# Performance work log

Measured on AMD Instinct MI355X. Metric: run time of the kernel, lower is better.

The kernel has to match this reference:

```python
import jax, jax.numpy as jnp
import numpy as np

D_MODEL = 1024
NUM_HEADS = 16
D_K = D_MODEL // NUM_HEADS  # 64
THETA = 10000.0


def apply_rope(x, positions, theta):
    # x: [b, h, s, d_k]; interleaved-pair RoPE
    d = x.shape[-1]
    inv_freq = theta ** (-jnp.arange(0, d, 2, dtype=jnp.float32) / d)  # [d/2]
    angles = positions.astype(jnp.float32)[:, None] * inv_freq[None, :]  # [s, d/2]
    cos = jnp.cos(angles)
    sin = jnp.sin(angles)
    x1 = x[..., 0::2]
    x2 = x[..., 1::2]
    out_even = x1 * cos - x2 * sin
    out_odd = x1 * sin + x2 * cos
    return jnp.stack([out_even, out_odd], axis=-1).reshape(x.shape)


def setup_inputs() -> dict:
    key = jax.random.key(0)
    kx, kq, kk, kv, ko = jax.random.split(key, 5)
    scale = 1.0 / np.sqrt(D_MODEL)
    return {
        "x": jax.random.normal(kx, (1, 4096, D_MODEL), dtype=jnp.float32),
        "Wq": jax.random.normal(kq, (D_MODEL, D_MODEL), dtype=jnp.float32) * scale,
        "Wk": jax.random.normal(kk, (D_MODEL, D_MODEL), dtype=jnp.float32) * scale,
        "Wv": jax.random.normal(kv, (D_MODEL, D_MODEL), dtype=jnp.float32) * scale,
        "Wo": jax.random.normal(ko, (D_MODEL, D_MODEL), dtype=jnp.float32) * scale,
    }


def reference(x, Wq, Wk, Wv, Wo):
    b, s, _ = x.shape
    # Linear (no bias, weight stored as [out, in]): y = x @ W^T
    q = jnp.einsum("bsd,ed->bse", x, Wq).reshape(b, s, NUM_HEADS, D_K).transpose(0, 2, 1, 3)
    k = jnp.einsum("bsd,ed->bse", x, Wk).reshape(b, s, NUM_HEADS, D_K).transpose(0, 2, 1, 3)
    v = jnp.einsum("bsd,ed->bse", x, Wv).reshape(b, s, NUM_HEADS, D_K).transpose(0, 2, 1, 3)

    positions = jnp.arange(s)
    q = apply_rope(q, positions, THETA)
    k = apply_rope(k, positions, THETA)

    scores = jnp.einsum("bhqd,bhkd->bhqk", q, k) / jnp.sqrt(jnp.float32(D_K))
    causal = jnp.tril(jnp.ones((s, s), dtype=bool))
    scores = jnp.where(causal, scores, -jnp.inf)
    probs = jax.nn.softmax(scores, axis=-1)
    ctx = jnp.einsum("bhqk,bhkd->bhqd", probs, v)  # [b,h,s,d_k]
    ctx = ctx.transpose(0, 2, 1, 3).reshape(b, s, D_MODEL)
    return jnp.einsum("bse,de->bsd", ctx, Wo)
```

## Files before the change

kernel.cpp:

```cpp
#include <hip/hip_runtime.h>
#include <hip/hip_bf16.h>
#include <math.h>


#define S_LEN 4096
#define DMODEL 1024
#define NHEAD 16
#define QSCALE 0.1803368801111244f

typedef __attribute__((ext_vector_type(8))) short short8;
typedef __attribute__((ext_vector_type(4))) short short4_t;
typedef __attribute__((ext_vector_type(4))) float floatx4;

static __device__ __forceinline__ void load_lds16(const void* g, void* l) {
    __builtin_amdgcn_global_load_lds((const __attribute__((address_space(1))) void*)g,
                                     (__attribute__((address_space(3))) void*)l, 16, 0, 0);
}

__global__ void cvt_all_kernel(const float* __restrict__ x,  const float* __restrict__ wq,
                               const float* __restrict__ wk, const float* __restrict__ wv,
                               const float* __restrict__ wo,
                               __hip_bfloat16* __restrict__ xb,  __hip_bfloat16* __restrict__ wqb,
                               __hip_bfloat16* __restrict__ wkb, __hip_bfloat16* __restrict__ wvb,
                               __hip_bfloat16* __restrict__ wob)
{
    const size_t NX = (size_t)S_LEN * DMODEL;
    const size_t NW = (size_t)DMODEL * DMODEL;
    size_t t = ((size_t)blockIdx.x * blockDim.x + threadIdx.x) * 4;
    const float* src; __hip_bfloat16* dst; size_t off;
    if (t < NX) { src = x; dst = xb; off = t; }
    else {
        size_t j = t - NX; int seg = (int)(j >> 20); off = j & (NW - 1);
        src = (seg == 0) ? wq : (seg == 1) ? wk : (seg == 2) ? wv : wo;
        dst = (seg == 0) ? wqb : (seg == 1) ? wkb : (seg == 2) ? wvb : wob;
    }
    float4 v = *(const float4*)(src + off);
    dst[off + 0] = __float2bfloat16(v.x);
    dst[off + 1] = __float2bfloat16(v.y);
    dst[off + 2] = __float2bfloat16(v.z);
    dst[off + 3] = __float2bfloat16(v.w);
}

__global__ __launch_bounds__(256) void qkv_gemm(
    const __hip_bfloat16* __restrict__ A,
    const __hip_bfloat16* __restrict__ Bq,
    const __hip_bfloat16* __restrict__ Bk,
    const __hip_bfloat16* __restrict__ Bv,
    __hip_bfloat16* __restrict__ Qb,
    __hip_bfloat16* __restrict__ Kb,
    __hip_bfloat16* __restrict__ Vtb)
{
    __shared__ __hip_bfloat16 As[128 * 32];
    __shared__ __hip_bfloat16 Bs[128 * 32];
    const int tid  = threadIdx.x;
    const int wave = tid >> 6;
    const int lane = tid & 63;
    const int quad = lane >> 4;
    const int l15  = lane & 15;
    const int sec  = blockIdx.x >> 3;
    const __hip_bfloat16* B = (sec == 0) ? Bq : (sec == 1) ? Bk : Bv;
    const int n0 = (blockIdx.x & 7) * 128;
    const int m0 = blockIdx.y * 128;
    const int wm = (wave & 1) * 64;
    const int wn = (wave >> 1) * 64;

    floatx4 acc[4][4] = {};

    for (int kt = 0; kt < DMODEL; kt += 32) {
        #pragma unroll
        for (int p = 0; p < 2; ++p) {
            int base = (p * 4 + wave) * 1024;
            int b    = base + lane * 16;
            int row  = b >> 6;
            int ke   = (b & 63) >> 1;
            load_lds16(A + (size_t)(m0 + row) * DMODEL + kt + ke, (char*)As + base);
            load_lds16(B + (size_t)(n0 + row) * DMODEL + kt + ke, (char*)Bs + base);
        }
        __syncthreads();
        short8 af[4], bf[4];
        #pragma unroll
        for (int i = 0; i < 4; ++i)
            af[i] = *(const short8*)(As + (wm + i * 16 + l15) * 32 + quad * 8);
        #pragma unroll
        for (int j = 0; j < 4; ++j)
            bf[j] = *(const short8*)(Bs + (wn + j * 16 + l15) * 32 + quad * 8);
        #pragma unroll
        for (int i = 0; i < 4; ++i)
            #pragma unroll
            for (int j = 0; j < 4; ++j)
                acc[i][j] = __builtin_amdgcn_mfma_f32_16x16x32_bf16(af[i], bf[j], acc[i][j], 0, 0, 0);
        __syncthreads();
    }

    float ifreq[4];
    #pragma unroll
    for (int j = 0; j < 4; ++j) {
        int d = (j * 16 + l15) & 63;
        ifreq[j] = expf(-(float)(d & ~1) * (9.210340371976184f / 64.0f));
    }
    const float scale = (sec == 0) ? QSCALE : 1.0f;
    __hip_bfloat16* dst = (sec == 0) ? Qb : Kb;
    #pragma unroll
    for (int i = 0; i < 4; ++i) {
        int rowb = m0 + wm + i * 16 + quad * 4;
        #pragma unroll
        for (int j = 0; j < 4; ++j) {
            int col = n0 + wn + j * 16 + l15;
            int h   = col >> 6;
            int hd  = col & 63;
            if (sec == 2) {
                union { short4_t v; __hip_bfloat16 b[4]; } pk;
                #pragma unroll
                for (int r = 0; r < 4; ++r) pk.b[r] = __float2bfloat16(acc[i][j][r]);
                int od = hd >> 4, lv = hd & 15;
                *(short4_t*)(Vtb + (size_t)h * 262144 +
                             (((od * 512 + (rowb >> 3)) * 16 + lv) << 3) + (rowb & 7)) = pk.v;
            } else {
                int g = hd >> 3, jj = hd & 7;
                #pragma unroll
                for (int r = 0; r < 4; ++r) {
                    int rr  = rowb + r;
                    float v = acc[i][j][r];
                    float ang = (float)rr * ifreq[j];
                    float sn, cs;
                    __sincosf(ang, &sn, &cs);
                    float pv  = __shfl_xor(v, 1);
                    float out = ((lane & 1) ? (pv * sn + v * cs)
                                            : (v * cs - pv * sn)) * scale;
                    dst[(size_t)h * 262144 +
                        ((((rr >> 4) * 8 + g) * 16 + (rr & 15)) << 3) + jj] = __float2bfloat16(out);
                }
            }
        }
    }
}

template<bool EDGE>
static __device__ __forceinline__ void attn_tile(
    int kt, int quad, int l15,
    const __hip_bfloat16* __restrict__ Kh, const __hip_bfloat16* __restrict__ Vh,
    const short8 aq[4][2], floatx4 o[4][4], float lp[4][4],
    __hip_bfloat16* __restrict__ PsW)
{
    asm volatile("s_waitcnt lgkmcnt(0)" ::: "memory");

    short8 kf[4][2], vf[4][2];
    #pragma unroll
    for (int ni = 0; ni < 4; ++ni)
        #pragma unroll
        for (int dc = 0; dc < 2; ++dc)
            kf[ni][dc] = *(const short8*)(Kh + (size_t)(((((kt*4 + ni)*8 + dc*4 + quad)*16 + l15) << 3)));
    #pragma unroll
    for (int od = 0; od < 4; ++od)
        #pragma unroll
        for (int dc = 0; dc < 2; ++dc)
            vf[od][dc] = *(const short8*)(Vh + (size_t)((((od*512 + kt*8 + dc*4 + quad)*16 + l15) << 3)));

    #pragma unroll
    for (int g = 0; g < 4; ++g) {
        floatx4 st[4];
        #pragma unroll
        for (int ni = 0; ni < 4; ++ni) {
            floatx4 z = {};
            floatx4 s = __builtin_amdgcn_mfma_f32_16x16x32_bf16(aq[g][0], kf[ni][0], z, 0, 0, 0);
            st[ni]    = __builtin_amdgcn_mfma_f32_16x16x32_bf16(aq[g][1], kf[ni][1], s, 0, 0, 0);
        }
        #pragma unroll
        for (int ni = 0; ni < 4; ++ni) {
            #pragma unroll
            for (int r = 0; r < 4; ++r) {
                float e = __builtin_amdgcn_exp2f(st[ni][r]);
                if (EDGE) {
                    if (ni * 16 + l15 > g * 16 + quad * 4 + r) e = 0.0f;
                }
                lp[g][r] += e;
                PsW[(g * 16 + quad * 4 + r) * 68 + ni * 16 + l15] = __float2bfloat16(e);
            }
        }
    }
    #pragma unroll
    for (int g = 0; g < 4; ++g) {
        short8 ap[2];
        #pragma unroll
        for (int dc = 0; dc < 2; ++dc) {
            const __hip_bfloat16* pp = PsW + (g * 16 + l15) * 68 + dc * 32 + quad * 8;
            short4_t p0 = *(const short4_t*)pp;
            short4_t p1 = *(const short4_t*)(pp + 4);
            short8 a;
            a[0] = p0[0]; a[1] = p0[1]; a[2] = p0[2]; a[3] = p0[3];
            a[4] = p1[0]; a[5] = p1[1]; a[6] = p1[2]; a[7] = p1[3];
            ap[dc] = a;
        }
        #pragma unroll
        for (int od = 0; od < 4; ++od) {
            o[g][od] = __builtin_amdgcn_mfma_f32_16x16x32_bf16(ap[0], vf[od][0], o[g][od], 0, 0, 0);
            o[g][od] = __builtin_amdgcn_mfma_f32_16x16x32_bf16(ap[1], vf[od][1], o[g][od], 0, 0, 0);
        }
    }
}

__global__ __launch_bounds__(256) void attn_kernel(
    const __hip_bfloat16* __restrict__ Q,
    const __hip_bfloat16* __restrict__ Kp,
    const __hip_bfloat16* __restrict__ Vp,
    __hip_bfloat16* __restrict__ CTX)
{
    __shared__ __hip_bfloat16 Buf[4][64 * 68];
    __shared__ float LPw[4][64];
    const int b  = blockIdx.x;
    const int h  = b & 15;
    const int u  = 63 - (b >> 4);
    const int tid  = threadIdx.x;
    const int wave = tid >> 6, lane = tid & 63;
    const int quad = lane >> 4, l15 = lane & 15;

    const __hip_bfloat16* Qh = Q  + (size_t)h * 262144;
    const __hip_bfloat16* Kh = Kp + (size_t)h * 262144;
    const __hip_bfloat16* Vh = Vp + (size_t)h * 262144;
    __hip_bfloat16* PsW = &Buf[wave][0];

    short8 aq[4][2];
    #pragma unroll
    for (int g = 0; g < 4; ++g)
        #pragma unroll
        for (int dc = 0; dc < 2; ++dc)
            aq[g][dc] = *(const short8*)(Qh + (size_t)(((((u*4 + g)*8 + dc*4 + quad)*16 + l15) << 3)));

    floatx4 o[4][4] = {};
    float lp[4][4] = {};

    for (int kt = wave; kt < u; kt += 4)
        attn_tile<false>(kt, quad, l15, Kh, Vh, aq, o, lp, PsW);
    if ((u & 3) == wave)
        attn_tile<true>(u, quad, l15, Kh, Vh, aq, o, lp, PsW);

    #pragma unroll
    for (int g = 0; g < 4; ++g)
        #pragma unroll
        for (int r = 0; r < 4; ++r) {
            float v = lp[g][r];
            v += __shfl_xor(v, 1);
            v += __shfl_xor(v, 2);
            v += __shfl_xor(v, 4);
            v += __shfl_xor(v, 8);
            lp[g][r] = v;
        }
    asm volatile("s_waitcnt lgkmcnt(0)" ::: "memory");
    if (l15 == 0) {
        #pragma unroll
        for (int g = 0; g < 4; ++g)
            #pragma unroll
            for (int r = 0; r < 4; ++r)
                LPw[wave][g * 16 + quad * 4 + r] = lp[g][r];
    }
    #pragma unroll
    for (int g = 0; g < 4; ++g)
        #pragma unroll
        for (int od = 0; od < 4; ++od)
            #pragma unroll
            for (int r = 0; r < 4; ++r)
                Buf[wave][(g * 16 + quad * 4 + r) * 68 + od * 16 + l15] =
                    __float2bfloat16(o[g][od][r]);
    __syncthreads();

    #pragma unroll
    for (int r = 0; r < 4; ++r) {
        int q = wave * 16 + quad * 4 + r;
        float ls = LPw[0][q] + LPw[1][q] + LPw[2][q] + LPw[3][q];
        float rl = __frcp_rn(ls);
        #pragma unroll
        for (int od = 0; od < 4; ++od) {
            float s = 0.0f;
            #pragma unroll
            for (int sl = 0; sl < 4; ++sl)
                s += __bfloat162float(Buf[sl][q * 68 + od * 16 + l15]);
            CTX[(size_t)(u * 64 + q) * DMODEL + h * 64 + od * 16 + l15] =
                __float2bfloat16(s * rl);
        }
    }
}

__global__ __launch_bounds__(256) void out_gemm(
    const __hip_bfloat16* __restrict__ A,
    const __hip_bfloat16* __restrict__ B,
    float* __restrict__ C)
{
    __shared__ __hip_bfloat16 As[128 * 32];
    __shared__ __hip_bfloat16 Bs[64 * 32];
    const int tid  = threadIdx.x;
    const int wave = tid >> 6;
    const int lane = tid & 63;
    const int quad = lane >> 4;
    const int l15  = lane & 15;
    const int n0 = blockIdx.x * 64;
    const int m0 = blockIdx.y * 128;
    const int wm = (wave & 1) * 64;
    const int wn = (wave >> 1) * 32;

    floatx4 acc[4][2] = {};

    for (int kt = 0; kt < DMODEL; kt += 32) {
        #pragma unroll
        for (int p = 0; p < 3; ++p) {
            int id  = p * 4 + wave;
            if (id < 8) {
                int base = id * 1024;
                int b    = base + lane * 16;
                int row  = b >> 6;
                int ke   = (b & 63) >> 1;
                load_lds16(A + (size_t)(m0 + row) * DMODEL + kt + ke, (char*)As + base);
            } else {
                int base = (id - 8) * 1024;
                int b    = base + lane * 16;
                int row  = b >> 6;
                int ke   = (b & 63) >> 1;
                load_lds16(B + (size_t)(n0 + row) * DMODEL + kt + ke, (char*)Bs + base);
            }
        }
        __syncthreads();
        short8 af[4], bf[2];
        #pragma unroll
        for (int i = 0; i < 4; ++i)
            af[i] = *(const short8*)(As + (wm + i * 16 + l15) * 32 + quad * 8);
        #pragma unroll
        for (int j = 0; j < 2; ++j)
            bf[j] = *(const short8*)(Bs + (wn + j * 16 + l15) * 32 + quad * 8);
        #pragma unroll
        for (int i = 0; i < 4; ++i)
            #pragma unroll
            for (int j = 0; j < 2; ++j)
                acc[i][j] = __builtin_amdgcn_mfma_f32_16x16x32_bf16(af[i], bf[j], acc[i][j], 0, 0, 0);
        __syncthreads();
    }

    #pragma unroll
    for (int i = 0; i < 4; ++i) {
        int rowb = m0 + wm + i * 16 + quad * 4;
        #pragma unroll
        for (int j = 0; j < 2; ++j) {
            int col = n0 + wn + j * 16 + l15;
            #pragma unroll
            for (int r = 0; r < 4; ++r)
                C[(size_t)(rowb + r) * DMODEL + col] = acc[i][j][r];
        }
    }
}

extern "C" void kernel_launch(void* const* d_in, const int* in_sizes, int n_in,
                              void* d_out, int out_size, void* d_ws, size_t ws_size,
                              hipStream_t stream)
{
    const float* x  = (const float*)d_in[0];
    const float* Wq = (const float*)d_in[1];
    const float* Wk = (const float*)d_in[2];
    const float* Wv = (const float*)d_in[3];
    const float* Wo = (const float*)d_in[4];

    char* ws = (char*)d_ws;
    const size_t MB = 1024 * 1024;
    __hip_bfloat16* xb  = (__hip_bfloat16*)(ws);
    __hip_bfloat16* wqb = (__hip_bfloat16*)(ws +  8 * MB);
    __hip_bfloat16* wkb = (__hip_bfloat16*)(ws + 10 * MB);
    __hip_bfloat16* wvb = (__hip_bfloat16*)(ws + 12 * MB);
    __hip_bfloat16* wob = (__hip_bfloat16*)(ws + 14 * MB);
    __hip_bfloat16* Qb  = (__hip_bfloat16*)(ws + 16 * MB);
    __hip_bfloat16* Kbf = (__hip_bfloat16*)(ws + 24 * MB);
    __hip_bfloat16* Vtb = (__hip_bfloat16*)(ws + 32 * MB);
    __hip_bfloat16* Cx  = (__hip_bfloat16*)(ws + 40 * MB);

    cvt_all_kernel<<<8192, 256, 0, stream>>>(x, Wq, Wk, Wv, Wo, xb, wqb, wkb, wvb, wob);

    qkv_gemm<<<dim3(24, 32), 256, 0, stream>>>(xb, wqb, wkb, wvb, Qb, Kbf, Vtb);

    attn_kernel<<<1024, 256, 0, stream>>>(Qb, Kbf, Vtb, Cx);

    out_gemm<<<dim3(16, 32), 256, 0, stream>>>(Cx, wob, (float*)d_out);
}
```

Before: 221.5 us.

## Transpose QK^T MFMA operands for packed P stores and fast bf16 rounding

The score MFMA now takes K and Q in swapped operand order. Each lane therefore holds four consecutive key columns for a single query row, so the probability tile is written to LDS as packed 8-byte stores into a padded stride-76 strip. The row-sum reduction shrinks to two cross-quad shuffles. A cheap round-half-up bf16 conversion replaces __float2bfloat16 in the converters, the GEMM epilogues and attention, and the attention kernel asks for two blocks per CU via launch bounds. The shortcut conversion skips NaN handling and round-to-even, which slightly changes numerics, and the occupancy hint may cause register spills.

```diff
diff --git a/kernel.cpp b/kernel.cpp
--- a/kernel.cpp
+++ b/kernel.cpp
@@ -7,14 +7,27 @@
 #define DMODEL 1024
 #define NHEAD 16
 #define QSCALE 0.1803368801111244f
+#define PSTR 76
 
 typedef __attribute__((ext_vector_type(8))) short short8;
 typedef __attribute__((ext_vector_type(4))) short short4_t;
+typedef __attribute__((ext_vector_type(2))) unsigned int uint2_t;
 typedef __attribute__((ext_vector_type(4))) float floatx4;
 
 static __device__ __forceinline__ void load_lds16(const void* g, void* l) {
     __builtin_amdgcn_global_load_lds((const __attribute__((address_space(1))) void*)g,
                                      (__attribute__((address_space(3))) void*)l, 16, 0, 0);
+}
+
+static __device__ __forceinline__ __hip_bfloat16 bf16_fast(float f) {
+    unsigned int u = __builtin_bit_cast(unsigned int, f) + 0x8000u;
+    unsigned short s = (unsigned short)(u >> 16);
+    return __builtin_bit_cast(__hip_bfloat16, s);
+}
+static __device__ __forceinline__ unsigned int pack_bf16x2(float a, float b) {
+    unsigned int ua = __builtin_bit_cast(unsigned int, a) + 0x8000u;
+    unsigned int ub = __builtin_bit_cast(unsigned int, b) + 0x8000u;
+    return __builtin_amdgcn_perm(ub, ua, 0x07060302);
 }
 
 __global__ void cvt_all_kernel(const float* __restrict__ x,  const float* __restrict__ wq,
@@ -35,10 +48,10 @@
         dst = (seg == 0) ? wqb : (seg == 1) ? wkb : (seg == 2) ? wvb : wob;
     }
     float4 v = *(const float4*)(src + off);
-    dst[off + 0] = __float2bfloat16(v.x);
-    dst[off + 1] = __float2bfloat16(v.y);
-    dst[off + 2] = __float2bfloat16(v.z);
-    dst[off + 3] = __float2bfloat16(v.w);
+    uint2_t w;
+    w.x = pack_bf16x2(v.x, v.y);
+    w.y = pack_bf16x2(v.z, v.w);
+    *(uint2_t*)(dst + off) = w;
 }
 
 __global__ __launch_bounds__(256) void qkv_gemm(
@@ -109,12 +122,12 @@
             int h   = col >> 6;
             int hd  = col & 63;
             if (sec == 2) {
-                union { short4_t v; __hip_bfloat16 b[4]; } pk;
-                #pragma unroll
-                for (int r = 0; r < 4; ++r) pk.b[r] = __float2bfloat16(acc[i][j][r]);
+                uint2_t w;
+                w.x = pack_bf16x2(acc[i][j][0], acc[i][j][1]);
+                w.y = pack_bf16x2(acc[i][j][2], acc[i][j][3]);
                 int od = hd >> 4, lv = hd & 15;
-                *(short4_t*)(Vtb + (size_t)h * 262144 +
-                             (((od * 512 + (rowb >> 3)) * 16 + lv) << 3) + (rowb & 7)) = pk.v;
+                *(uint2_t*)(Vtb + (size_t)h * 262144 +
+                            (((od * 512 + (rowb >> 3)) * 16 + lv) << 3) + (rowb & 7)) = w;
             } else {
                 int g = hd >> 3, jj = hd & 7;
                 #pragma unroll
@@ -128,7 +141,7 @@
                     float out = ((lane & 1) ? (pv * sn + v * cs)
                                             : (v * cs - pv * sn)) * scale;
                     dst[(size_t)h * 262144 +
-                        ((((rr >> 4) * 8 + g) * 16 + (rr & 15)) << 3) + jj] = __float2bfloat16(out);
+                        ((((rr >> 4) * 8 + g) * 16 + (rr & 15)) << 3) + jj] = bf16_fast(out);
                 }
             }
         }
@@ -139,7 +152,7 @@
 static __device__ __forceinline__ void attn_tile(
     int kt, int quad, int l15,
     const __hip_bfloat16* __restrict__ Kh, const __hip_bfloat16* __restrict__ Vh,
-    const short8 aq[4][2], floatx4 o[4][4], float lp[4][4],
+    const short8 aq[4][2], floatx4 o[4][4], float lp[4],
     __hip_bfloat16* __restrict__ PsW)
 {
     asm volatile("s_waitcnt lgkmcnt(0)" ::: "memory");
@@ -158,32 +171,35 @@
 
     #pragma unroll
     for (int g = 0; g < 4; ++g) {
+        __hip_bfloat16* strip = PsW + (g * 16 + l15) * PSTR;
         floatx4 st[4];
         #pragma unroll
         for (int ni = 0; ni < 4; ++ni) {
             floatx4 z = {};
-            floatx4 s = __builtin_amdgcn_mfma_f32_16x16x32_bf16(aq[g][0], kf[ni][0], z, 0, 0, 0);
-            st[ni]    = __builtin_amdgcn_mfma_f32_16x16x32_bf16(aq[g][1], kf[ni][1], s, 0, 0, 0);
+            floatx4 s = __builtin_amdgcn_mfma_f32_16x16x32_bf16(kf[ni][0], aq[g][0], z, 0, 0, 0);
+            st[ni]    = __builtin_amdgcn_mfma_f32_16x16x32_bf16(kf[ni][1], aq[g][1], s, 0, 0, 0);
         }
         #pragma unroll
         for (int ni = 0; ni < 4; ++ni) {
+            float e[4];
             #pragma unroll
             for (int r = 0; r < 4; ++r) {
-                float e = __builtin_amdgcn_exp2f(st[ni][r]);
+                float v = __builtin_amdgcn_exp2f(st[ni][r]);
                 if (EDGE) {
-                    if (ni * 16 + l15 > g * 16 + quad * 4 + r) e = 0.0f;
+                    if (ni * 16 + quad * 4 + r > g * 16 + l15) v = 0.0f;
                 }
-                lp[g][r] += e;
-                PsW[(g * 16 + quad * 4 + r) * 68 + ni * 16 + l15] = __float2bfloat16(e);
+                e[r] = v;
             }
-        }
-    }
-    #pragma unroll
-    for (int g = 0; g < 4; ++g) {
+            lp[g] += (e[0] + e[1]) + (e[2] + e[3]);
+            uint2_t w;
+            w.x = pack_bf16x2(e[0], e[1]);
+            w.y = pack_bf16x2(e[2], e[3]);
+            *(short4_t*)(strip + ni * 16 + quad * 4) = __builtin_bit_cast(short4_t, w);
+        }
         short8 ap[2];
         #pragma unroll
         for (int dc = 0; dc < 2; ++dc) {
-            const __hip_bfloat16* pp = PsW + (g * 16 + l15) * 68 + dc * 32 + quad * 8;
+            const __hip_bfloat16* pp = strip + dc * 32 + quad * 8;
             short4_t p0 = *(const short4_t*)pp;
             short4_t p1 = *(const short4_t*)(pp + 4);
             short8 a;
@@ -199,13 +215,13 @@
     }
 }
 
-__global__ __launch_bounds__(256) void attn_kernel(
+__global__ __launch_bounds__(256, 2) void attn_kernel(
     const __hip_bfloat16* __restrict__ Q,
     const __hip_bfloat16* __restrict__ Kp,
     const __hip_bfloat16* __restrict__ Vp,
     __hip_bfloat16* __restrict__ CTX)
 {
-    __shared__ __hip_bfloat16 Buf[4][64 * 68];
+    __shared__ __hip_bfloat16 Buf[4][64 * PSTR];
     __shared__ float LPw[4][64];
     const int b  = blockIdx.x;
     const int h  = b & 15;
@@ -227,7 +243,7 @@
             aq[g][dc] = *(const short8*)(Qh + (size_t)(((((u*4 + g)*8 + dc*4 + quad)*16 + l15) << 3)));
 
     floatx4 o[4][4] = {};
-    float lp[4][4] = {};
+    float lp[4] = {};
 
     for (int kt = wave; kt < u; kt += 4)
         attn_tile<false>(kt, quad, l15, Kh, Vh, aq, o, lp, PsW);
@@ -235,32 +251,26 @@
         attn_tile<true>(u, quad, l15, Kh, Vh, aq, o, lp, PsW);
 
     #pragma unroll
+    for (int g = 0; g < 4; ++g) {
+        float v = lp[g];
+        v += __shfl_xor(v, 16);
+        v += __shfl_xor(v, 32);
+        lp[g] = v;
+    }
+    asm volatile("s_waitcnt lgkmcnt(0)" ::: "memory");
+    if (quad == 0) {
+        #pragma unroll
+        for (int g = 0; g < 4; ++g)
+            LPw[wave][g * 16 + l15] = lp[g];
+    }
+    #pragma unroll
     for (int g = 0; g < 4; ++g)
         #pragma unroll
-        for (int r = 0; r < 4; ++r) {
-            float v = lp[g][r];
-            v += __shfl_xor(v, 1);
-            v += __shfl_xor(v, 2);
-            v += __shfl_xor(v, 4);
-            v += __shfl_xor(v, 8);
-            lp[g][r] = v;
-        }
-    asm volatile("s_waitcnt lgkmcnt(0)" ::: "memory");
-    if (l15 == 0) {
-        #pragma unroll
-        for (int g = 0; g < 4; ++g)
+        for (int od = 0; od < 4; ++od)
             #pragma unroll
             for (int r = 0; r < 4; ++r)
-                LPw[wave][g * 16 + quad * 4 + r] = lp[g][r];
-    }
-    #pragma unroll
-    for (int g = 0; g < 4; ++g)
-        #pragma unroll
-        for (int od = 0; od < 4; ++od)
-            #pragma unroll
-            for (int r = 0; r < 4; ++r)
-                Buf[wave][(g * 16 + quad * 4 + r) * 68 + od * 16 + l15] =
-                    __float2bfloat16(o[g][od][r]);
+                Buf[wave][(g * 16 + quad * 4 + r) * PSTR + od * 16 + l15] =
+                    bf16_fast(o[g][od][r]);
     __syncthreads();
 
     #pragma unroll
@@ -273,9 +283,9 @@
             float s = 0.0f;
             #pragma unroll
             for (int sl = 0; sl < 4; ++sl)
-                s += __bfloat162float(Buf[sl][q * 68 + od * 16 + l15]);
+                s += __bfloat162float(Buf[sl][q * PSTR + od * 16 + l15]);
             CTX[(size_t)(u * 64 + q) * DMODEL + h * 64 + od * 16 + l15] =
-                __float2bfloat16(s * rl);
+                bf16_fast(s * rl);
         }
     }
 }
```

After: 202.4 us. 1.09x faster.
